# Kernel tuning notes

Hardware: AMD Instinct MI355X
Metric: run time of the kernel (lower is better)

Reference implementation:

```python
import jax, jax.numpy as jnp
import numpy as np

TOP_K = 32
OBS_RADIUS = 1.0
N = 4096
IN_DIM = 4


def setup_inputs() -> dict:
    key = jax.random.key(0)
    ks = jax.random.split(key, 10)
    s = 0.05
    return {
        "states": jax.random.normal(ks[0], (N, 4), jnp.float32),
        "goals": jax.random.normal(ks[1], (N, 2), jnp.float32),
        "W1": jax.random.normal(ks[2], (64, IN_DIM + 1), jnp.float32) * s,
        "b1": jnp.zeros((64,), jnp.float32),
        "W2": jax.random.normal(ks[3], (128, 64), jnp.float32) * s,
        "b2": jnp.zeros((128,), jnp.float32),
        "Wd1": jax.random.normal(ks[4], (64, 132), jnp.float32) * s,
        "bd1": jnp.zeros((64,), jnp.float32),
        "Wd2": jax.random.normal(ks[5], (128, 64), jnp.float32) * s,
        "bd2": jnp.zeros((128,), jnp.float32),
        "Wd3": jax.random.normal(ks[6], (64, 128), jnp.float32) * s,
        "bd3": jnp.zeros((64,), jnp.float32),
        "Wd4": jax.random.normal(ks[7], (4, 64), jnp.float32) * s,
        "bd4": jnp.zeros((4,), jnp.float32),
    }


def reference(states, goals, W1, b1, W2, b2, Wd1, bd1, Wd2, bd2, Wd3, bd3, Wd4, bd4):
    n = states.shape[0]
    dt = states.dtype
    # pairwise relative states + one-hot self indicator -> [N, N, 5]
    x = states[:, None, :] - states[None, :, :]
    x = jnp.concatenate([x, jnp.eye(n, dtype=dt)[:, :, None]], axis=2)
    # remove_distant_agents: keep TOP_K nearest neighbors by planar distance
    d = jnp.sqrt(jnp.sum(x[:, :, :2] ** 2, axis=2) + 1e-4)  # [N, N]
    _, idx = jax.lax.top_k(-d, TOP_K)                        # [N, K]
    xk = jnp.take_along_axis(x, idx[:, :, None], axis=1)     # [N, K, 5]
    # observation-radius mask (torch reshape [N,K,1]->[N,1,K] == transpose here)
    dist = jnp.linalg.norm(xk[:, :, :2], axis=2)             # [N, K]
    mask = (dist < OBS_RADIUS).astype(dt).reshape(n, 1, TOP_K)
    # NOTE: original uses a raw reshape [N,K,5]->[N,5,K] (not a transpose); match it
    h = xk.reshape(n, IN_DIM + 1, TOP_K)
    # pointwise (kernel-1) conv stack 5 -> 64 -> 128
    h = jax.nn.relu(jnp.einsum('oc,ncp->nop', W1, h) + b1[None, :, None])
    h = jax.nn.relu(jnp.einsum('oc,ncp->nop', W2, h) + b2[None, :, None])
    # original does torch.max(...)[1]: ARGMAX indices, promoted to float by cat
    x_local = jnp.argmax(h * mask, axis=2).astype(dt)        # [N, 128]
    rel = states[:, :2] - goals
    feat = jnp.concatenate([x_local, rel, states[:, 2:]], axis=1)  # [N, 132]
    z = jax.nn.relu(feat @ Wd1.T + bd1)
    z = jax.nn.relu(z @ Wd2.T + bd2)
    z = jax.nn.relu(z @ Wd3.T + bd3)
    z = z @ Wd4.T + bd4
    k = 2.0 * jax.nn.sigmoid(z) + 0.2                        # [N, 4] gains
    state = jnp.concatenate([rel, states[:, 2:]], axis=1)    # [N, 4]
    a_x = -(k[:, 0] * state[:, 0] + k[:, 1] * state[:, 2])
    a_y = -(k[:, 2] * state[:, 1] + k[:, 3] * state[:, 3])
    return jnp.stack([a_x, a_y], axis=1)                     # [N, 2]
```

## Files before the change

### kernel.cpp

```cpp
#include <hip/hip_runtime.h>
#include <math.h>

#define NAGENT 4096
#define TOPK 32
#define FAGB 8
#define CANDCAP 2048

__global__ __launch_bounds__(256) void topk_kernel(
    const float* __restrict__ states, int* __restrict__ idx_out)
{
    const int i = blockIdx.x;
    const int t = threadIdx.x;
    const int lane = t & 63;
    __shared__ unsigned int hist[1024];
    __shared__ unsigned int wsum[4];
    __shared__ unsigned long long cand[CANDCAP];
    __shared__ int ccount;
    __shared__ unsigned int cutB;

    #pragma unroll
    for (int u = 0; u < 4; ++u) hist[t + u * 256] = 0u;
    if (t == 0) ccount = 0;

    const float4 si = ((const float4*)states)[i];
    __syncthreads();

    unsigned int mybits[16];
    #pragma unroll
    for (int u = 0; u < 16; ++u) {
        int j = t + u * 256;
        float4 sj = ((const float4*)states)[j];
        float dx = __fsub_rn(si.x, sj.x);
        float dy = __fsub_rn(si.y, sj.y);
        float s  = __fadd_rn(__fadd_rn(__fmul_rn(dx, dx), __fmul_rn(dy, dy)), 1e-4f);
        float dv = sqrtf(s);
        mybits[u] = __float_as_uint(dv);
        unsigned int bin = (unsigned int)(dv * 256.0f);
        if (bin > 1023u) bin = 1023u;
        atomicAdd(&hist[bin], 1u);
    }
    __syncthreads();

    unsigned int h0 = hist[t * 4 + 0], h1 = hist[t * 4 + 1];
    unsigned int h2 = hist[t * 4 + 2], h3 = hist[t * 4 + 3];
    unsigned int v = h0 + h1 + h2 + h3;
    unsigned int inc = v;
    #pragma unroll
    for (int off = 1; off < 64; off <<= 1) {
        unsigned int u = __shfl_up(inc, off, 64);
        if (lane >= off) inc += u;
    }
    if (lane == 63) wsum[t >> 6] = inc;
    __syncthreads();
    unsigned int woff = 0;
    for (int w = 0; w < (t >> 6); ++w) woff += wsum[w];
    unsigned int incl = inc + woff;
    unsigned int exc  = incl - v;
    if (exc < TOPK && incl >= TOPK) {
        unsigned int cum = exc;
        unsigned int hh[4] = {h0, h1, h2, h3};
        int b = t * 4 + 3;
        #pragma unroll
        for (int q = 0; q < 4; ++q) {
            cum += hh[q];
            if (cum >= TOPK) { b = t * 4 + q; break; }
        }
        cutB = (unsigned int)b;
    }
    __syncthreads();

    const unsigned int B = cutB;
    #pragma unroll
    for (int u = 0; u < 16; ++u) {
        float dv = __uint_as_float(mybits[u]);
        unsigned int bin = (unsigned int)(dv * 256.0f);
        if (bin > 1023u) bin = 1023u;
        if (bin <= B) {
            int pos = atomicAdd(&ccount, 1);
            if (pos < CANDCAP)
                cand[pos] = ((unsigned long long)mybits[u] << 32)
                          | (unsigned int)(t + u * 256);
        }
    }
    __syncthreads();

    const int C = (ccount < CANDCAP) ? ccount : CANDCAP;
    for (int q = t; q < C; q += 256) {
        unsigned long long key = cand[q];
        int rank = 0;
        for (int r = 0; r < C; ++r) rank += (cand[r] < key) ? 1 : 0;
        if (rank < TOPK) idx_out[i * TOPK + rank] = (int)(key & 0xffffffffu);
    }
}

__global__ __launch_bounds__(512, 2) void fused_kernel(
    const float* __restrict__ states, const float* __restrict__ goals,
    const float* __restrict__ W1,  const float* __restrict__ b1,
    const float* __restrict__ W2,  const float* __restrict__ b2,
    const float* __restrict__ Wd1, const float* __restrict__ bd1,
    const float* __restrict__ Wd2, const float* __restrict__ bd2,
    const float* __restrict__ Wd3, const float* __restrict__ bd3,
    const float* __restrict__ Wd4, const float* __restrict__ bd4,
    const int* __restrict__ idx_in, float* __restrict__ out)
{
    const int t = threadIdx.x;
    const int a = t >> 6;
    const int l = t & 63;
    const int base = blockIdx.x * FAGB;
    const int i = base + a;

    __shared__ __attribute__((aligned(16))) float w2a[64 * 68];
    __shared__ __attribute__((aligned(16))) float w2b[64 * 68];
    __shared__ __attribute__((aligned(16))) float w1s[320];
    __shared__ __attribute__((aligned(16))) float b1s[64];
    __shared__ __attribute__((aligned(16))) float b2s[128];
    __shared__ __attribute__((aligned(16))) float flat[8][160];
    __shared__ __attribute__((aligned(16))) float maskv[8][32];
    __shared__ __attribute__((aligned(16))) float featb[8][132];
    __shared__ __attribute__((aligned(16))) float h1p[8][1024];

    if (l < 32) {
        int j = idx_in[i * TOPK + l];
        float4 sj  = ((const float4*)states)[j];
        float4 siv = ((const float4*)states)[i];
        float d0 = siv.x - sj.x;
        float d1 = siv.y - sj.y;
        float d2 = siv.z - sj.z;
        float d3 = siv.w - sj.w;
        flat[a][l * 5 + 0] = d0;
        flat[a][l * 5 + 1] = d1;
        flat[a][l * 5 + 2] = d2;
        flat[a][l * 5 + 3] = d3;
        flat[a][l * 5 + 4] = (j == i) ? 1.0f : 0.0f;
        float dist = sqrtf(__fadd_rn(__fmul_rn(d0, d0), __fmul_rn(d1, d1)));
        maskv[a][l] = (dist < 1.0f) ? 1.0f : 0.0f;
    } else if (l < 36) {
        int f = l - 32;
        float4 siv = ((const float4*)states)[i];
        float2 gi  = ((const float2*)goals)[i];
        float v = (f == 0) ? (siv.x - gi.x)
                : (f == 1) ? (siv.y - gi.y)
                : (f == 2) ? siv.z : siv.w;
        featb[a][128 + f] = v;
    }

    #pragma unroll
    for (int u = 0; u < 16; ++u) {
        int e = t + u * 512;
        int o = e >> 6, c = e & 63;
        float v = W2[e];
        int dst = c * 68 + ((o >> 3) << 2) + (o & 3);
        if (o & 4) w2b[dst] = v; else w2a[dst] = v;
    }
    if (t < 320) w1s[t] = W1[t];
    if (t < 64)  b1s[t] = b1[t];
    if (t < 128) b2s[t] = b2[t];
    __syncthreads();

    const int ow = l & 15;
    const int ph = l >> 4;

    float bb[8];
    #pragma unroll
    for (int k = 0; k < 8; ++k) bb[k] = b2s[ow * 8 + k];

    unsigned long long rbest[8];
    #pragma unroll
    for (int k = 0; k < 8; ++k) rbest[k] = 0ull;

    #pragma unroll
    for (int pq = 0; pq < 2; ++pq) {
        #pragma unroll
        for (int u = 0; u < 16; ++u) {
            int e = u * 64 + l;
            int o1 = e >> 4, pp = e & 15;
            float acc = b1s[o1];
            #pragma unroll
            for (int f = 0; f < 5; ++f)
                acc += w1s[o1 * 5 + f] * flat[a][f * 32 + pq * 16 + pp];
            h1p[a][e] = fmaxf(acc, 0.0f);
        }

        float4 mv4 = *(const float4*)&maskv[a][pq * 16 + ph * 4];
        float mv[4] = {mv4.x, mv4.y, mv4.z, mv4.w};

        float acc[8][4];
        #pragma unroll
        for (int k = 0; k < 8; ++k)
            #pragma unroll
            for (int q = 0; q < 4; ++q) acc[k][q] = 0.0f;

        for (int c4 = 0; c4 < 16; ++c4) {
            float4 wAv[4], wBv[4], hv[4];
            #pragma unroll
            for (int cc = 0; cc < 4; ++cc) {
                int c = c4 * 4 + cc;
                wAv[cc] = *(const float4*)&w2a[c * 68 + ow * 4];
                wBv[cc] = *(const float4*)&w2b[c * 68 + ow * 4];
                hv[cc]  = *(const float4*)&h1p[a][c * 16 + ph * 4];
            }
            #pragma unroll
            for (int cc = 0; cc < 4; ++cc) {
                float wv[8] = {wAv[cc].x, wAv[cc].y, wAv[cc].z, wAv[cc].w,
                               wBv[cc].x, wBv[cc].y, wBv[cc].z, wBv[cc].w};
                float hq[4] = {hv[cc].x, hv[cc].y, hv[cc].z, hv[cc].w};
                #pragma unroll
                for (int k = 0; k < 8; ++k)
                    #pragma unroll
                    for (int q = 0; q < 4; ++q)
                        acc[k][q] += wv[k] * hq[q];
            }
        }

        #pragma unroll
        for (int k = 0; k < 8; ++k) {
            unsigned long long best = rbest[k];
            #pragma unroll
            for (int q = 0; q < 4; ++q) {
                float val = fmaxf(acc[k][q] + bb[k], 0.0f) * mv[q];
                int p = pq * 16 + ph * 4 + q;
                unsigned long long key =
                    ((unsigned long long)__float_as_uint(val) << 32)
                    | (unsigned int)(31 - p);
                if (key > best) best = key;
            }
            rbest[k] = best;
        }
    }

    #pragma unroll
    for (int k = 0; k < 8; ++k) {
        unsigned long long best = rbest[k];
        unsigned long long o1 = __shfl_xor(best, 16, 64); if (o1 > best) best = o1;
        unsigned long long o2 = __shfl_xor(best, 32, 64); if (o2 > best) best = o2;
        if (ph == 0) {
            int pbest = 31 - (int)(best & 63ull);
            featb[a][ow * 8 + k] = (float)pbest;
        }
    }

    float* z1s = &h1p[a][0];
    float* z2s = z1s + 64;
    float* z3s = z1s + 192;
    float* kvs = z1s + 256;

    {
        float a0 = bd1[l];
        for (int k = 0; k < 33; ++k) {
            float4 wv = *(const float4*)&Wd1[l * 132 + 4 * k];
            float4 f0 = *(const float4*)&featb[a][4 * k];
            a0 += wv.x * f0.x; a0 += wv.y * f0.y; a0 += wv.z * f0.z; a0 += wv.w * f0.w;
        }
        z1s[l] = fmaxf(a0, 0.0f);
    }

    {
        float accA = bd2[l];
        float accB = bd2[l + 64];
        for (int k = 0; k < 16; ++k) {
            float4 wa = *(const float4*)&Wd2[l * 64 + 4 * k];
            float4 wb = *(const float4*)&Wd2[(l + 64) * 64 + 4 * k];
            float4 f0 = *(const float4*)&z1s[4 * k];
            accA += wa.x * f0.x; accA += wa.y * f0.y;
            accA += wa.z * f0.z; accA += wa.w * f0.w;
            accB += wb.x * f0.x; accB += wb.y * f0.y;
            accB += wb.z * f0.z; accB += wb.w * f0.w;
        }
        z2s[l]      = fmaxf(accA, 0.0f);
        z2s[l + 64] = fmaxf(accB, 0.0f);
    }

    {
        float a0 = bd3[l];
        for (int k = 0; k < 32; ++k) {
            float4 wv = *(const float4*)&Wd3[l * 128 + 4 * k];
            float4 f0 = *(const float4*)&z2s[4 * k];
            a0 += wv.x * f0.x; a0 += wv.y * f0.y; a0 += wv.z * f0.z; a0 += wv.w * f0.w;
        }
        z3s[l] = fmaxf(a0, 0.0f);
    }

    if (l < 4) {
        float acc = bd4[l];
        for (int c = 0; c < 64; ++c) acc += Wd4[l * 64 + c] * z3s[c];
        kvs[l] = 2.0f / (1.0f + expf(-acc)) + 0.2f;
    }
    if (l < 2) {
        float ka = kvs[2 * l + 0];
        float kb = kvs[2 * l + 1];
        float rel = featb[a][128 + l];
        float vel = featb[a][130 + l];
        out[i * 2 + l] = -(ka * rel + kb * vel);
    }
}

extern "C" void kernel_launch(void* const* d_in, const int* in_sizes, int n_in,
                              void* d_out, int out_size, void* d_ws, size_t ws_size,
                              hipStream_t stream)
{
    const float* states = (const float*)d_in[0];
    const float* goals  = (const float*)d_in[1];
    const float* W1  = (const float*)d_in[2];
    const float* b1  = (const float*)d_in[3];
    const float* W2  = (const float*)d_in[4];
    const float* b2  = (const float*)d_in[5];
    const float* Wd1 = (const float*)d_in[6];
    const float* bd1 = (const float*)d_in[7];
    const float* Wd2 = (const float*)d_in[8];
    const float* bd2 = (const float*)d_in[9];
    const float* Wd3 = (const float*)d_in[10];
    const float* bd3 = (const float*)d_in[11];
    const float* Wd4 = (const float*)d_in[12];
    const float* bd4 = (const float*)d_in[13];

    int*   idx = (int*)d_ws;
    float* out = (float*)d_out;

    topk_kernel<<<NAGENT, 256, 0, stream>>>(states, idx);
    fused_kernel<<<NAGENT / FAGB, 512, 0, stream>>>(states, goals, W1, b1, W2, b2,
                                                    Wd1, bd1, Wd2, bd2, Wd3, bd3,
                                                    Wd4, bd4, idx, out);
}
```

Before: 158.9 us.

## Restructure fused MLP kernel: per-lane neighbor h1 in registers, DPP wave max for argmax

Reorganizes the fused kernel so each lane owns one neighbor point, holds its 64-wide first-layer activations in registers, and loops over output channels reading W2 rows directly from global or constant memory instead of staging W2 in LDS. The argmax over the 32 neighbors is done with DPP row max steps plus a shuffle and a ballot/ffs to find the first matching index, replacing the 64-bit packed key compare and shuffles. The block shrinks to 256 threads handling 4 agents, which cuts LDS use substantially to allow more occupancy. The costs are 64 live registers per lane for h1, serialized per-output reductions (64 iterations each with cross-lane ops), and weight reads that are uniform but not reused from LDS.

Result: slower. 255.6 us (+60.9%).

```diff
diff --git a/kernel.cpp b/kernel.cpp
--- a/kernel.cpp
+++ b/kernel.cpp
@@ -3,7 +3,6 @@
 
 #define NAGENT 4096
 #define TOPK 32
-#define FAGB 8
 #define CANDCAP 2048
 
 __global__ __launch_bounds__(256) void topk_kernel(
@@ -93,7 +92,14 @@
     }
 }
 
-__global__ __launch_bounds__(512, 2) void fused_kernel(
+template <int CTRL>
+__device__ __forceinline__ float dpp_max_step(float x)
+{
+    int y = __builtin_amdgcn_update_dpp(0, __float_as_int(x), CTRL, 0xF, 0xF, true);
+    return fmaxf(x, __int_as_float(y));
+}
+
+__global__ __launch_bounds__(256, 4) void fused_kernel(
     const float* __restrict__ states, const float* __restrict__ goals,
     const float* __restrict__ W1,  const float* __restrict__ b1,
     const float* __restrict__ W2,  const float* __restrict__ b2,
@@ -104,151 +110,94 @@
     const int* __restrict__ idx_in, float* __restrict__ out)
 {
     const int t = threadIdx.x;
-    const int a = t >> 6;
+    const int w = t >> 6;
     const int l = t & 63;
-    const int base = blockIdx.x * FAGB;
-    const int i = base + a;
-
-    __shared__ __attribute__((aligned(16))) float w2a[64 * 68];
-    __shared__ __attribute__((aligned(16))) float w2b[64 * 68];
-    __shared__ __attribute__((aligned(16))) float w1s[320];
-    __shared__ __attribute__((aligned(16))) float b1s[64];
-    __shared__ __attribute__((aligned(16))) float b2s[128];
-    __shared__ __attribute__((aligned(16))) float flat[8][160];
-    __shared__ __attribute__((aligned(16))) float maskv[8][32];
-    __shared__ __attribute__((aligned(16))) float featb[8][132];
-    __shared__ __attribute__((aligned(16))) float h1p[8][1024];
-
-    if (l < 32) {
-        int j = idx_in[i * TOPK + l];
-        float4 sj  = ((const float4*)states)[j];
-        float4 siv = ((const float4*)states)[i];
-        float d0 = siv.x - sj.x;
-        float d1 = siv.y - sj.y;
-        float d2 = siv.z - sj.z;
-        float d3 = siv.w - sj.w;
-        flat[a][l * 5 + 0] = d0;
-        flat[a][l * 5 + 1] = d1;
-        flat[a][l * 5 + 2] = d2;
-        flat[a][l * 5 + 3] = d3;
-        flat[a][l * 5 + 4] = (j == i) ? 1.0f : 0.0f;
-        float dist = sqrtf(__fadd_rn(__fmul_rn(d0, d0), __fmul_rn(d1, d1)));
-        maskv[a][l] = (dist < 1.0f) ? 1.0f : 0.0f;
-    } else if (l < 36) {
-        int f = l - 32;
-        float4 siv = ((const float4*)states)[i];
-        float2 gi  = ((const float2*)goals)[i];
-        float v = (f == 0) ? (siv.x - gi.x)
-                : (f == 1) ? (siv.y - gi.y)
-                : (f == 2) ? siv.z : siv.w;
-        featb[a][128 + f] = v;
-    }
-
-    #pragma unroll
-    for (int u = 0; u < 16; ++u) {
-        int e = t + u * 512;
-        int o = e >> 6, c = e & 63;
-        float v = W2[e];
-        int dst = c * 68 + ((o >> 3) << 2) + (o & 3);
-        if (o & 4) w2b[dst] = v; else w2a[dst] = v;
-    }
-    if (t < 320) w1s[t] = W1[t];
-    if (t < 64)  b1s[t] = b1[t];
-    if (t < 128) b2s[t] = b2[t];
-    __syncthreads();
-
-    const int ow = l & 15;
-    const int ph = l >> 4;
-
-    float bb[8];
-    #pragma unroll
-    for (int k = 0; k < 8; ++k) bb[k] = b2s[ow * 8 + k];
-
-    unsigned long long rbest[8];
-    #pragma unroll
-    for (int k = 0; k < 8; ++k) rbest[k] = 0ull;
-
-    #pragma unroll
-    for (int pq = 0; pq < 2; ++pq) {
+    const int pair  = w >> 1;
+    const int obase = (w & 1) << 6;
+    const int half  = l >> 5;
+    const int fa    = pair * 2 + half;
+    const int g     = blockIdx.x * 4 + fa;
+    const int p     = l & 31;
+
+    __shared__ __attribute__((aligned(16))) float flat[4][160];
+    __shared__ __attribute__((aligned(16))) float featb[4][132];
+    __shared__ __attribute__((aligned(16))) float zpool[4][264];
+
+    int j = idx_in[g * TOPK + p];
+    float4 sj = ((const float4*)states)[j];
+    float4 si = ((const float4*)states)[g];
+    float d0 = si.x - sj.x;
+    float d1 = si.y - sj.y;
+    float d2 = si.z - sj.z;
+    float d3 = si.w - sj.w;
+    float slf = (j == g) ? 1.0f : 0.0f;
+    float dist = sqrtf(__fadd_rn(__fmul_rn(d0, d0), __fmul_rn(d1, d1)));
+    float mask = (dist < 1.0f) ? 1.0f : 0.0f;
+
+    flat[fa][p * 5 + 0] = d0;
+    flat[fa][p * 5 + 1] = d1;
+    flat[fa][p * 5 + 2] = d2;
+    flat[fa][p * 5 + 3] = d3;
+    flat[fa][p * 5 + 4] = slf;
+
+    if (p < 4) {
+        float2 gi = ((const float2*)goals)[g];
+        float v = (p == 0) ? (si.x - gi.x)
+                : (p == 1) ? (si.y - gi.y)
+                : (p == 2) ? si.z : si.w;
+        featb[fa][128 + p] = v;
+    }
+    __syncthreads();
+
+    float in5[5];
+    #pragma unroll
+    for (int f = 0; f < 5; ++f) in5[f] = flat[fa][f * 32 + p];
+
+    float h1reg[64];
+    #pragma unroll
+    for (int c = 0; c < 64; ++c) {
+        float acc = b1[c];
         #pragma unroll
-        for (int u = 0; u < 16; ++u) {
-            int e = u * 64 + l;
-            int o1 = e >> 4, pp = e & 15;
-            float acc = b1s[o1];
-            #pragma unroll
-            for (int f = 0; f < 5; ++f)
-                acc += w1s[o1 * 5 + f] * flat[a][f * 32 + pq * 16 + pp];
-            h1p[a][e] = fmaxf(acc, 0.0f);
-        }
-
-        float4 mv4 = *(const float4*)&maskv[a][pq * 16 + ph * 4];
-        float mv[4] = {mv4.x, mv4.y, mv4.z, mv4.w};
-
-        float acc[8][4];
+        for (int f = 0; f < 5; ++f)
+            acc += W1[c * 5 + f] * in5[f];
+        h1reg[c] = fmaxf(acc, 0.0f);
+    }
+
+    for (int oi = 0; oi < 64; ++oi) {
+        const int o = obase + oi;
+        const float* __restrict__ w2r = &W2[o * 64];
+        float acc = 0.0f;
         #pragma unroll
-        for (int k = 0; k < 8; ++k)
-            #pragma unroll
-            for (int q = 0; q < 4; ++q) acc[k][q] = 0.0f;
-
-        for (int c4 = 0; c4 < 16; ++c4) {
-            float4 wAv[4], wBv[4], hv[4];
-            #pragma unroll
-            for (int cc = 0; cc < 4; ++cc) {
-                int c = c4 * 4 + cc;
-                wAv[cc] = *(const float4*)&w2a[c * 68 + ow * 4];
-                wBv[cc] = *(const float4*)&w2b[c * 68 + ow * 4];
-                hv[cc]  = *(const float4*)&h1p[a][c * 16 + ph * 4];
-            }
-            #pragma unroll
-            for (int cc = 0; cc < 4; ++cc) {
-                float wv[8] = {wAv[cc].x, wAv[cc].y, wAv[cc].z, wAv[cc].w,
-                               wBv[cc].x, wBv[cc].y, wBv[cc].z, wBv[cc].w};
-                float hq[4] = {hv[cc].x, hv[cc].y, hv[cc].z, hv[cc].w};
-                #pragma unroll
-                for (int k = 0; k < 8; ++k)
-                    #pragma unroll
-                    for (int q = 0; q < 4; ++q)
-                        acc[k][q] += wv[k] * hq[q];
-            }
-        }
-
-        #pragma unroll
-        for (int k = 0; k < 8; ++k) {
-            unsigned long long best = rbest[k];
-            #pragma unroll
-            for (int q = 0; q < 4; ++q) {
-                float val = fmaxf(acc[k][q] + bb[k], 0.0f) * mv[q];
-                int p = pq * 16 + ph * 4 + q;
-                unsigned long long key =
-                    ((unsigned long long)__float_as_uint(val) << 32)
-                    | (unsigned int)(31 - p);
-                if (key > best) best = key;
-            }
-            rbest[k] = best;
-        }
-    }
-
-    #pragma unroll
-    for (int k = 0; k < 8; ++k) {
-        unsigned long long best = rbest[k];
-        unsigned long long o1 = __shfl_xor(best, 16, 64); if (o1 > best) best = o1;
-        unsigned long long o2 = __shfl_xor(best, 32, 64); if (o2 > best) best = o2;
-        if (ph == 0) {
-            int pbest = 31 - (int)(best & 63ull);
-            featb[a][ow * 8 + k] = (float)pbest;
-        }
-    }
-
-    float* z1s = &h1p[a][0];
+        for (int c = 0; c < 64; ++c)
+            acc += w2r[c] * h1reg[c];
+        float val = fmaxf(acc + b2[o], 0.0f) * mask;
+
+        float m = val;
+        m = dpp_max_step<0xB1>(m);
+        m = dpp_max_step<0x4E>(m);
+        m = dpp_max_step<0x141>(m);
+        m = dpp_max_step<0x140>(m);
+        m = fmaxf(m, __shfl_xor(m, 16, 64));
+
+        unsigned long long bal = __ballot(val == m);
+        unsigned int bh = half ? (unsigned int)(bal >> 32) : (unsigned int)bal;
+        float pb = (float)(__ffs(bh) - 1);
+        if (p == 0) featb[fa][o] = pb;
+    }
+
+    __syncthreads();
+
+    float* z1s = &zpool[w][0];
     float* z2s = z1s + 64;
     float* z3s = z1s + 192;
     float* kvs = z1s + 256;
+    const int gd = blockIdx.x * 4 + w;
 
     {
         float a0 = bd1[l];
         for (int k = 0; k < 33; ++k) {
             float4 wv = *(const float4*)&Wd1[l * 132 + 4 * k];
-            float4 f0 = *(const float4*)&featb[a][4 * k];
+            float4 f0 = *(const float4*)&featb[w][4 * k];
             a0 += wv.x * f0.x; a0 += wv.y * f0.y; a0 += wv.z * f0.z; a0 += wv.w * f0.w;
         }
         z1s[l] = fmaxf(a0, 0.0f);
@@ -288,9 +237,9 @@
     if (l < 2) {
         float ka = kvs[2 * l + 0];
         float kb = kvs[2 * l + 1];
-        float rel = featb[a][128 + l];
-        float vel = featb[a][130 + l];
-        out[i * 2 + l] = -(ka * rel + kb * vel);
+        float rel = featb[w][128 + l];
+        float vel = featb[w][130 + l];
+        out[gd * 2 + l] = -(ka * rel + kb * vel);
     }
 }
 
@@ -317,7 +266,7 @@
     float* out = (float*)d_out;
 
     topk_kernel<<<NAGENT, 256, 0, stream>>>(states, idx);
-    fused_kernel<<<NAGENT / FAGB, 512, 0, stream>>>(states, goals, W1, b1, W2, b2,
-                                                    Wd1, bd1, Wd2, bd2, Wd3, bd3,
-                                                    Wd4, bd4, idx, out);
-}
+    fused_kernel<<<NAGENT / 4, 256, 0, stream>>>(states, goals, W1, b1, W2, b2,
+                                                 Wd1, bd1, Wd2, bd2, Wd3, bd3,
+                                                 Wd4, bd4, idx, out);
+}
```

## Read transposed W2 from global in fused kernel, shrink blocks, use 16-bit indices

Applied to the files above, without the earlier changes.

The topk kernel's first block now writes a transposed copy of W2 to workspace. The fused kernel reads W2 straight from global/L2 instead of staging it in shared memory, which frees about 35KB of LDS per block. The fused kernel now uses 4 agents per 256-thread block and computes all 32 positions in one 8x8 register tile rather than two 8x4 passes. Neighbour indices are stored as 16-bit values to cut workspace traffic. The trade-offs are more global weight loads per wave and more registers for the 64-entry accumulator.

Result: slower. 162.7 us (+2.4%).

```diff
diff --git a/kernel.cpp b/kernel.cpp
--- a/kernel.cpp
+++ b/kernel.cpp
@@ -3,11 +3,11 @@
 
 #define NAGENT 4096
 #define TOPK 32
-#define FAGB 8
 #define CANDCAP 2048
 
 __global__ __launch_bounds__(256) void topk_kernel(
-    const float* __restrict__ states, int* __restrict__ idx_out)
+    const float* __restrict__ states, const float* __restrict__ W2,
+    unsigned short* __restrict__ idx_out, float* __restrict__ w2t)
 {
     const int i = blockIdx.x;
     const int t = threadIdx.x;
@@ -17,6 +17,13 @@
     __shared__ unsigned long long cand[CANDCAP];
     __shared__ int ccount;
     __shared__ unsigned int cutB;
+
+    if (i == 0) {
+        for (int e = t; e < 8192; e += 256) {
+            int o = e & 127, c = e >> 7;
+            w2t[c * 128 + o] = W2[o * 64 + c];
+        }
+    }
 
     #pragma unroll
     for (int u = 0; u < 4; ++u) hist[t + u * 256] = 0u;
@@ -89,157 +96,131 @@
         unsigned long long key = cand[q];
         int rank = 0;
         for (int r = 0; r < C; ++r) rank += (cand[r] < key) ? 1 : 0;
-        if (rank < TOPK) idx_out[i * TOPK + rank] = (int)(key & 0xffffffffu);
+        if (rank < TOPK)
+            idx_out[i * TOPK + rank] = (unsigned short)(key & 0xffffu);
     }
 }
 
-__global__ __launch_bounds__(512, 2) void fused_kernel(
+__global__ __launch_bounds__(256) void fused_kernel(
     const float* __restrict__ states, const float* __restrict__ goals,
     const float* __restrict__ W1,  const float* __restrict__ b1,
-    const float* __restrict__ W2,  const float* __restrict__ b2,
+    const float* __restrict__ w2t, const float* __restrict__ b2,
     const float* __restrict__ Wd1, const float* __restrict__ bd1,
     const float* __restrict__ Wd2, const float* __restrict__ bd2,
     const float* __restrict__ Wd3, const float* __restrict__ bd3,
     const float* __restrict__ Wd4, const float* __restrict__ bd4,
-    const int* __restrict__ idx_in, float* __restrict__ out)
+    const unsigned short* __restrict__ idx_in, float* __restrict__ out)
 {
     const int t = threadIdx.x;
-    const int a = t >> 6;
+    const int w = t >> 6;
     const int l = t & 63;
-    const int base = blockIdx.x * FAGB;
-    const int i = base + a;
-
-    __shared__ __attribute__((aligned(16))) float w2a[64 * 68];
-    __shared__ __attribute__((aligned(16))) float w2b[64 * 68];
+    const int g = blockIdx.x * 4 + w;
+
     __shared__ __attribute__((aligned(16))) float w1s[320];
     __shared__ __attribute__((aligned(16))) float b1s[64];
     __shared__ __attribute__((aligned(16))) float b2s[128];
-    __shared__ __attribute__((aligned(16))) float flat[8][160];
-    __shared__ __attribute__((aligned(16))) float maskv[8][32];
-    __shared__ __attribute__((aligned(16))) float featb[8][132];
-    __shared__ __attribute__((aligned(16))) float h1p[8][1024];
+    __shared__ __attribute__((aligned(16))) float flat[4][160];
+    __shared__ __attribute__((aligned(16))) float maskv[4][32];
+    __shared__ __attribute__((aligned(16))) float featb[4][132];
+    __shared__ __attribute__((aligned(16))) float h1[4][2048];
 
     if (l < 32) {
-        int j = idx_in[i * TOPK + l];
+        int j = (int)idx_in[g * TOPK + l];
         float4 sj  = ((const float4*)states)[j];
-        float4 siv = ((const float4*)states)[i];
+        float4 siv = ((const float4*)states)[g];
         float d0 = siv.x - sj.x;
         float d1 = siv.y - sj.y;
         float d2 = siv.z - sj.z;
         float d3 = siv.w - sj.w;
-        flat[a][l * 5 + 0] = d0;
-        flat[a][l * 5 + 1] = d1;
-        flat[a][l * 5 + 2] = d2;
-        flat[a][l * 5 + 3] = d3;
-        flat[a][l * 5 + 4] = (j == i) ? 1.0f : 0.0f;
+        flat[w][l * 5 + 0] = d0;
+        flat[w][l * 5 + 1] = d1;
+        flat[w][l * 5 + 2] = d2;
+        flat[w][l * 5 + 3] = d3;
+        flat[w][l * 5 + 4] = (j == g) ? 1.0f : 0.0f;
         float dist = sqrtf(__fadd_rn(__fmul_rn(d0, d0), __fmul_rn(d1, d1)));
-        maskv[a][l] = (dist < 1.0f) ? 1.0f : 0.0f;
+        maskv[w][l] = (dist < 1.0f) ? 1.0f : 0.0f;
     } else if (l < 36) {
         int f = l - 32;
-        float4 siv = ((const float4*)states)[i];
-        float2 gi  = ((const float2*)goals)[i];
+        float4 siv = ((const float4*)states)[g];
+        float2 gi  = ((const float2*)goals)[g];
         float v = (f == 0) ? (siv.x - gi.x)
                 : (f == 1) ? (siv.y - gi.y)
                 : (f == 2) ? siv.z : siv.w;
-        featb[a][128 + f] = v;
-    }
-
-    #pragma unroll
-    for (int u = 0; u < 16; ++u) {
-        int e = t + u * 512;
-        int o = e >> 6, c = e & 63;
-        float v = W2[e];
-        int dst = c * 68 + ((o >> 3) << 2) + (o & 3);
-        if (o & 4) w2b[dst] = v; else w2a[dst] = v;
-    }
-    if (t < 320) w1s[t] = W1[t];
+        featb[w][128 + f] = v;
+    }
+
+    for (int e = t; e < 320; e += 256) w1s[e] = W1[e];
     if (t < 64)  b1s[t] = b1[t];
     if (t < 128) b2s[t] = b2[t];
     __syncthreads();
 
+    #pragma unroll
+    for (int u = 0; u < 32; ++u) {
+        int e = u * 64 + l;
+        int p = e & 31, o1 = e >> 5;
+        float acc = b1s[o1];
+        #pragma unroll
+        for (int f = 0; f < 5; ++f)
+            acc += w1s[o1 * 5 + f] * flat[w][f * 32 + p];
+        h1[w][o1 * 32 + p] = fmaxf(acc, 0.0f);
+    }
+
     const int ow = l & 15;
-    const int ph = l >> 4;
-
-    float bb[8];
-    #pragma unroll
-    for (int k = 0; k < 8; ++k) bb[k] = b2s[ow * 8 + k];
-
-    unsigned long long rbest[8];
-    #pragma unroll
-    for (int k = 0; k < 8; ++k) rbest[k] = 0ull;
-
-    #pragma unroll
-    for (int pq = 0; pq < 2; ++pq) {
-        #pragma unroll
-        for (int u = 0; u < 16; ++u) {
-            int e = u * 64 + l;
-            int o1 = e >> 4, pp = e & 15;
-            float acc = b1s[o1];
+    const int pt = l >> 4;
+    float acc[8][8];
+    #pragma unroll
+    for (int k = 0; k < 8; ++k)
+        #pragma unroll
+        for (int q = 0; q < 8; ++q) acc[k][q] = 0.0f;
+
+    for (int c4 = 0; c4 < 16; ++c4) {
+        float4 wAv[4], wBv[4], hAv[4], hBv[4];
+        #pragma unroll
+        for (int cc = 0; cc < 4; ++cc) {
+            int c = c4 * 4 + cc;
+            wAv[cc] = *(const float4*)&w2t[c * 128 + ow * 8];
+            wBv[cc] = *(const float4*)&w2t[c * 128 + ow * 8 + 4];
+            hAv[cc] = *(const float4*)&h1[w][c * 32 + pt * 8];
+            hBv[cc] = *(const float4*)&h1[w][c * 32 + pt * 8 + 4];
+        }
+        #pragma unroll
+        for (int cc = 0; cc < 4; ++cc) {
+            float wv[8] = {wAv[cc].x, wAv[cc].y, wAv[cc].z, wAv[cc].w,
+                           wBv[cc].x, wBv[cc].y, wBv[cc].z, wBv[cc].w};
+            float hv[8] = {hAv[cc].x, hAv[cc].y, hAv[cc].z, hAv[cc].w,
+                           hBv[cc].x, hBv[cc].y, hBv[cc].z, hBv[cc].w};
             #pragma unroll
-            for (int f = 0; f < 5; ++f)
-                acc += w1s[o1 * 5 + f] * flat[a][f * 32 + pq * 16 + pp];
-            h1p[a][e] = fmaxf(acc, 0.0f);
-        }
-
-        float4 mv4 = *(const float4*)&maskv[a][pq * 16 + ph * 4];
-        float mv[4] = {mv4.x, mv4.y, mv4.z, mv4.w};
-
-        float acc[8][4];
-        #pragma unroll
-        for (int k = 0; k < 8; ++k)
-            #pragma unroll
-            for (int q = 0; q < 4; ++q) acc[k][q] = 0.0f;
-
-        for (int c4 = 0; c4 < 16; ++c4) {
-            float4 wAv[4], wBv[4], hv[4];
-            #pragma unroll
-            for (int cc = 0; cc < 4; ++cc) {
-                int c = c4 * 4 + cc;
-                wAv[cc] = *(const float4*)&w2a[c * 68 + ow * 4];
-                wBv[cc] = *(const float4*)&w2b[c * 68 + ow * 4];
-                hv[cc]  = *(const float4*)&h1p[a][c * 16 + ph * 4];
-            }
-            #pragma unroll
-            for (int cc = 0; cc < 4; ++cc) {
-                float wv[8] = {wAv[cc].x, wAv[cc].y, wAv[cc].z, wAv[cc].w,
-                               wBv[cc].x, wBv[cc].y, wBv[cc].z, wBv[cc].w};
-                float hq[4] = {hv[cc].x, hv[cc].y, hv[cc].z, hv[cc].w};
+            for (int k = 0; k < 8; ++k)
                 #pragma unroll
-                for (int k = 0; k < 8; ++k)
-                    #pragma unroll
-                    for (int q = 0; q < 4; ++q)
-                        acc[k][q] += wv[k] * hq[q];
-            }
-        }
-
-        #pragma unroll
-        for (int k = 0; k < 8; ++k) {
-            unsigned long long best = rbest[k];
-            #pragma unroll
-            for (int q = 0; q < 4; ++q) {
-                float val = fmaxf(acc[k][q] + bb[k], 0.0f) * mv[q];
-                int p = pq * 16 + ph * 4 + q;
-                unsigned long long key =
-                    ((unsigned long long)__float_as_uint(val) << 32)
-                    | (unsigned int)(31 - p);
-                if (key > best) best = key;
-            }
-            rbest[k] = best;
-        }
-    }
-
+                for (int q = 0; q < 8; ++q)
+                    acc[k][q] += wv[k] * hv[q];
+        }
+    }
+
+    float4 mA = *(const float4*)&maskv[w][pt * 8];
+    float4 mB = *(const float4*)&maskv[w][pt * 8 + 4];
+    float mv[8] = {mA.x, mA.y, mA.z, mA.w, mB.x, mB.y, mB.z, mB.w};
     #pragma unroll
     for (int k = 0; k < 8; ++k) {
-        unsigned long long best = rbest[k];
+        float bb = b2s[ow * 8 + k];
+        unsigned long long best = 0ull;
+        #pragma unroll
+        for (int q = 0; q < 8; ++q) {
+            float val = fmaxf(acc[k][q] + bb, 0.0f) * mv[q];
+            unsigned long long key =
+                ((unsigned long long)__float_as_uint(val) << 32)
+                | (unsigned int)(31 - (pt * 8 + q));
+            if (key > best) best = key;
+        }
         unsigned long long o1 = __shfl_xor(best, 16, 64); if (o1 > best) best = o1;
         unsigned long long o2 = __shfl_xor(best, 32, 64); if (o2 > best) best = o2;
-        if (ph == 0) {
+        if (pt == 0) {
             int pbest = 31 - (int)(best & 63ull);
-            featb[a][ow * 8 + k] = (float)pbest;
-        }
-    }
-
-    float* z1s = &h1p[a][0];
+            featb[w][ow * 8 + k] = (float)pbest;
+        }
+    }
+
+    float* z1s = &h1[w][0];
     float* z2s = z1s + 64;
     float* z3s = z1s + 192;
     float* kvs = z1s + 256;
@@ -248,7 +229,7 @@
         float a0 = bd1[l];
         for (int k = 0; k < 33; ++k) {
             float4 wv = *(const float4*)&Wd1[l * 132 + 4 * k];
-            float4 f0 = *(const float4*)&featb[a][4 * k];
+            float4 f0 = *(const float4*)&featb[w][4 * k];
             a0 += wv.x * f0.x; a0 += wv.y * f0.y; a0 += wv.z * f0.z; a0 += wv.w * f0.w;
         }
         z1s[l] = fmaxf(a0, 0.0f);
@@ -281,16 +262,16 @@
     }
 
     if (l < 4) {
-        float acc = bd4[l];
-        for (int c = 0; c < 64; ++c) acc += Wd4[l * 64 + c] * z3s[c];
-        kvs[l] = 2.0f / (1.0f + expf(-acc)) + 0.2f;
+        float acc2 = bd4[l];
+        for (int c = 0; c < 64; ++c) acc2 += Wd4[l * 64 + c] * z3s[c];
+        kvs[l] = 2.0f / (1.0f + expf(-acc2)) + 0.2f;
     }
     if (l < 2) {
         float ka = kvs[2 * l + 0];
         float kb = kvs[2 * l + 1];
-        float rel = featb[a][128 + l];
-        float vel = featb[a][130 + l];
-        out[i * 2 + l] = -(ka * rel + kb * vel);
+        float rel = featb[w][128 + l];
+        float vel = featb[w][130 + l];
+        out[g * 2 + l] = -(ka * rel + kb * vel);
     }
 }
 
@@ -313,11 +294,12 @@
     const float* Wd4 = (const float*)d_in[12];
     const float* bd4 = (const float*)d_in[13];
 
-    int*   idx = (int*)d_ws;
+    unsigned short* idx = (unsigned short*)d_ws;
+    float* w2t = (float*)((char*)d_ws + NAGENT * TOPK * sizeof(unsigned short));
     float* out = (float*)d_out;
 
-    topk_kernel<<<NAGENT, 256, 0, stream>>>(states, idx);
-    fused_kernel<<<NAGENT / FAGB, 512, 0, stream>>>(states, goals, W1, b1, W2, b2,
-                                                    Wd1, bd1, Wd2, bd2, Wd3, bd3,
-                                                    Wd4, bd4, idx, out);
+    topk_kernel<<<NAGENT, 256, 0, stream>>>(states, W2, idx, w2t);
+    fused_kernel<<<NAGENT / 4, 256, 0, stream>>>(states, goals, W1, b1, w2t, b2,
+                                                 Wd1, bd1, Wd2, bd2, Wd3, bd3,
+                                                 Wd4, bd4, idx, out);
 }
```
